# Optimization experiments

Hardware: AMD Instinct MI355X
Metric: run time of the kernel (lower is better)

The kernel has to match this reference:

```python
import jax, jax.numpy as jnp
import numpy as np

N, E, D, H, EDIM, FIN = 16384, 65536, 512, 4, 4, 7
C = D  # per-head out channels (concat=False)


def seg_softmax(logits, seg, n):
    # numerically stable softmax over edges grouped by destination node
    m = jax.ops.segment_max(logits, seg, num_segments=n)
    e = jnp.exp(logits - m[seg])
    s = jax.ops.segment_sum(e, seg, num_segments=n)
    return e / (s[seg] + 1e-16)


def layer_norm(h, g, b):
    mu = h.mean(-1, keepdims=True)
    var = h.var(-1, keepdims=True)
    return (h - mu) / jnp.sqrt(var + 1e-5) * g + b


def setup_inputs() -> dict:
    key = jax.random.key(0)
    ks = jax.random.split(key, 24)
    f32 = jnp.float32
    nrm = lambda k, shp, s=0.05: jax.random.normal(k, shp, dtype=f32) * s
    inp = {}
    inp['x'] = jax.random.normal(ks[0], (N, FIN), dtype=f32)
    inp['edge_index'] = jax.random.randint(ks[1], (2, E), 0, N)
    inp['edge_attr'] = jax.random.uniform(ks[2], (E, EDIM), dtype=f32)
    # input projection
    inp['Wproj'] = nrm(ks[3], (FIN, D)); inp['bproj'] = jnp.zeros((D,), f32)
    # GINEConv (eps=0): edge lin + 2-layer MLP (512->1024->512)
    inp['gine_edge_W'] = nrm(ks[4], (EDIM, D)); inp['gine_edge_b'] = jnp.zeros((D,), f32)
    inp['gine_W1'] = nrm(ks[5], (D, 2 * D)); inp['gine_b1'] = jnp.zeros((2 * D,), f32)
    inp['gine_W2'] = nrm(ks[6], (2 * D, D)); inp['gine_b2'] = jnp.zeros((D,), f32)
    # GATv2Conv heads=4, concat=False
    inp['gat_Wl'] = nrm(ks[7], (D, H * C)); inp['gat_bl'] = jnp.zeros((H * C,), f32)
    inp['gat_Wr'] = nrm(ks[8], (D, H * C)); inp['gat_br'] = jnp.zeros((H * C,), f32)
    inp['gat_edge_W'] = nrm(ks[9], (EDIM, H * C))
    inp['gat_att'] = nrm(ks[10], (H, C))
    inp['gat_bias'] = jnp.zeros((D,), f32)
    # two GCNConv layers
    inp['gcn1_W'] = nrm(ks[11], (D, D)); inp['gcn1_b'] = jnp.zeros((D,), f32)
    inp['gcn2_W'] = nrm(ks[12], (D, D)); inp['gcn2_b'] = jnp.zeros((D,), f32)
    # 4 LayerNorms
    inp['ln_gamma'] = jnp.ones((4, D), f32)
    inp['ln_beta'] = jnp.zeros((4, D), f32)
    return inp


def _forward(x, edge_attr, Wproj, bproj, gine_edge_W, gine_edge_b, gine_W1, gine_b1,
             gine_W2, gine_b2, gat_Wl, gat_bl, gat_Wr, gat_br, gat_edge_W, gat_att,
             gat_bias, gcn1_W, gcn1_b, gcn2_W, gcn2_b, ln_gamma, ln_beta, edge_index):
    n = x.shape[0]
    src, dst = edge_index[0], edge_index[1]
    h = jax.nn.relu(x @ Wproj + bproj)

    # ---- layer 0: GINEConv, sum_j relu(x_j + lin_e(e_ij)), eps=0 ----
    res = h
    e = edge_attr @ gine_edge_W + gine_edge_b                      # [E, D]
    m = jax.nn.relu(h[src] + e)
    agg = jax.ops.segment_sum(m, dst, num_segments=n)              # [N, D]
    g = h + agg
    g = jax.nn.relu(g @ gine_W1 + gine_b1) @ gine_W2 + gine_b2
    h = layer_norm(jax.nn.relu(g) + res, ln_gamma[0], ln_beta[0])

    # ---- layer 1: GATv2Conv (heads=4, concat=False, self-loops, edge_dim=4) ----
    res = h
    loop = jnp.arange(n)
    src2 = jnp.concatenate([src, loop])
    dst2 = jnp.concatenate([dst, loop])
    mean_attr = edge_attr.mean(0)                                  # fill_value='mean'
    eattr2 = jnp.concatenate(
        [edge_attr, jnp.broadcast_to(mean_attr, (n, edge_attr.shape[1]))], 0)
    nh, nc = gat_att.shape
    xl = (h @ gat_Wl + gat_bl).reshape(n, nh, nc)                  # source transform
    xr = (h @ gat_Wr + gat_br).reshape(n, nh, nc)                  # target transform
    ee = (eattr2 @ gat_edge_W).reshape(-1, nh, nc)
    z = jax.nn.leaky_relu(xl[src2] + xr[dst2] + ee, 0.2)           # [E2, H, C]
    logits = jnp.einsum('ehc,hc->eh', z, gat_att)                  # [E2, H]
    alpha = seg_softmax(logits, dst2, n)
    out = jax.ops.segment_sum(xl[src2] * alpha[..., None], dst2, num_segments=n)
    g = out.mean(1) + gat_bias                                     # concat=False -> mean
    h = layer_norm(jax.nn.relu(g) + res, ln_gamma[1], ln_beta[1])

    # ---- layers 2,3: GCNConv (self-loops + symmetric norm) ----
    deg = jax.ops.segment_sum(jnp.ones_like(dst2, dtype=h.dtype), dst2, num_segments=n)
    dinv = jax.lax.rsqrt(deg)
    norm = dinv[src2] * dinv[dst2]
    for i, (W, b) in enumerate(((gcn1_W, gcn1_b), (gcn2_W, gcn2_b)), start=2):
        res = h
        hw = h @ W
        g = jax.ops.segment_sum(hw[src2] * norm[:, None], dst2, num_segments=n) + b
        h = layer_norm(jax.nn.relu(g) + res, ln_gamma[i], ln_beta[i])
    return h


def reference(x, edge_index, edge_attr, Wproj, bproj, gine_edge_W, gine_edge_b,
              gine_W1, gine_b1, gine_W2, gine_b2, gat_Wl, gat_bl, gat_Wr, gat_br,
              gat_edge_W, gat_att, gat_bias, gcn1_W, gcn1_b, gcn2_W, gcn2_b,
              ln_gamma, ln_beta):
    return _forward(x, edge_attr, Wproj, bproj, gine_edge_W, gine_edge_b, gine_W1,
                    gine_b1, gine_W2, gine_b2, gat_Wl, gat_bl, gat_Wr, gat_br,
                    gat_edge_W, gat_att, gat_bias, gcn1_W, gcn1_b, gcn2_W, gcn2_b,
                    ln_gamma, ln_beta, edge_index)
```

## Files before the change

### kernel.cpp

```cpp
#include <hip/hip_runtime.h>
#include <hip/hip_bf16.h>
#include <math.h>

#define NN   16384
#define EE   65536
#define DD   512
#define HH   4
#define FINN 7

typedef __attribute__((ext_vector_type(4))) float  floatx4;
typedef __attribute__((ext_vector_type(8))) float  floatx8;
typedef __attribute__((ext_vector_type(8))) short  shortx8;
typedef __attribute__((ext_vector_type(8))) unsigned short ushortx8;

__device__ inline float bf2f(unsigned short u) {
  return __uint_as_float(((unsigned)u) << 16);
}
__device__ inline unsigned short f2bf(float f) {
  unsigned u = __float_as_uint(f);
  unsigned r = (u + 0x7fffu + ((u >> 16) & 1u)) >> 16;
  return (unsigned short)r;
}
__device__ inline float wave_reduce_sum(float v) {
  #pragma unroll
  for (int off = 32; off > 0; off >>= 1) v += __shfl_down(v, off, 64);
  return v;
}
__device__ inline float wave_allreduce_sum(float v) {
  #pragma unroll
  for (int off = 32; off > 0; off >>= 1) v += __shfl_xor(v, off, 64);
  return v;
}
__device__ inline void async16(const unsigned short* g, unsigned short* l) {
  __builtin_amdgcn_global_load_lds(
      (const __attribute__((address_space(1))) void*)g,
      (__attribute__((address_space(3))) void*)l, 16, 0, 0);
}

__global__ void k_count(const int* __restrict__ dst, int* __restrict__ cnt) {
  int e = blockIdx.x * 256 + threadIdx.x;
  if (e < EE) atomicAdd(&cnt[dst[e]], 1);
}

__global__ void k_scan(const int* __restrict__ cnt, int* __restrict__ offs) {
  __shared__ int sums[256];
  int t = threadIdx.x;
  const int chunk = NN / 256;
  int base = t * chunk;
  int s = 0;
  for (int i = 0; i < chunk; ++i) s += cnt[base + i];
  sums[t] = s;
  __syncthreads();
  for (int off = 1; off < 256; off <<= 1) {
    int v = (t >= off) ? sums[t - off] : 0;
    __syncthreads();
    sums[t] += v;
    __syncthreads();
  }
  int run = (t == 0) ? 0 : sums[t - 1];
  for (int i = 0; i < chunk; ++i) {
    offs[base + i] = run;
    run += cnt[base + i];
  }
  if (t == 255) offs[NN] = run;
}

__global__ void k_fill(const int* __restrict__ dst, const int* __restrict__ offs,
                       int* __restrict__ cursor, int* __restrict__ eids) {
  int e = blockIdx.x * 256 + threadIdx.x;
  if (e >= EE) return;
  int d = dst[e];
  int p = offs[d] + atomicAdd(&cursor[d], 1);
  eids[p] = e;
}

__global__ void k_edge_mean(const float* __restrict__ eattr, float* __restrict__ macc) {
  int tid = blockIdx.x * blockDim.x + threadIdx.x;
  int stride = gridDim.x * blockDim.x;
  float ax = 0.f, ay = 0.f, az = 0.f, aw = 0.f;
  for (int e = tid; e < EE; e += stride) {
    float4 v = ((const float4*)eattr)[e];
    ax += v.x; ay += v.y; az += v.z; aw += v.w;
  }
  ax = wave_reduce_sum(ax); ay = wave_reduce_sum(ay);
  az = wave_reduce_sum(az); aw = wave_reduce_sum(aw);
  if ((threadIdx.x & 63) == 0) {
    atomicAdd(&macc[0], ax); atomicAdd(&macc[1], ay);
    atomicAdd(&macc[2], az); atomicAdd(&macc[3], aw);
  }
}

__global__ void k_transcast(const float* __restrict__ W, int ld,
                            unsigned short* __restrict__ Wt, int K, int N) {
  __shared__ float tile[32][33];
  int bx = blockIdx.x;
  int by = blockIdx.y;
  int tx = threadIdx.x & 31, ty = threadIdx.x >> 5;
  #pragma unroll
  for (int i = 0; i < 32; i += 8)
    tile[ty + i][tx] = W[(size_t)(by * 32 + ty + i) * ld + bx * 32 + tx];
  __syncthreads();
  #pragma unroll
  for (int i = 0; i < 32; i += 8)
    Wt[(size_t)(bx * 32 + ty + i) * K + by * 32 + tx] = f2bf(tile[tx][ty + i]);
}

__global__ void k_bcomb(const float* __restrict__ bl, const float* __restrict__ br,
                        float* __restrict__ bc0, float* __restrict__ bc1) {
  int i = blockIdx.x * 256 + threadIdx.x;
  if (i >= 4096) return;
  int b = i >> 11, c = i & 2047;
  float v = (c < 1024) ? bl[b * 1024 + c] : br[b * 1024 + c - 1024];
  (b ? bc1 : bc0)[c] = v;
}

__global__ void k_proj(const float* __restrict__ x, const float* __restrict__ W,
                       const float* __restrict__ b, unsigned short* __restrict__ hbf) {
  int gid = blockIdx.x * 256 + threadIdx.x;
  if (gid >= NN * DD) return;
  int n = gid >> 9, d = gid & 511;
  const float* xr = x + n * FINN;
  float acc = b[d];
  #pragma unroll
  for (int k = 0; k < FINN; ++k) acc = fmaf(xr[k], W[k * DD + d], acc);
  hbf[gid] = f2bf(fmaxf(acc, 0.f));
}

__global__ __launch_bounds__(256) void k_bgemm(
    const unsigned short* __restrict__ A, const unsigned short* __restrict__ Bt,
    const float* __restrict__ bias, void* __restrict__ Cout,
    int M, int Nc, int K, int act, int outbf) {
  __shared__ unsigned short As[128 * 64];
  __shared__ unsigned short Bs[128 * 64];
  const int tid = threadIdx.x;
  const int wv = tid >> 6;
  const int lane = tid & 63;
  const int row0 = blockIdx.y * 128;
  const int col0 = blockIdx.x * 128;
  const int wrow = (wv & 1) * 64;
  const int wcol = (wv >> 1) * 64;

  floatx4 acc[4][4];
  #pragma unroll
  for (int r = 0; r < 4; ++r)
    #pragma unroll
    for (int c = 0; c < 4; ++c)
      #pragma unroll
      for (int q = 0; q < 4; ++q) acc[r][c][q] = 0.f;

  const unsigned short* Ab = A + (size_t)row0 * K;
  const unsigned short* Bb = Bt + (size_t)col0 * K;
  const int lrow = lane >> 3;
  const int lchunk = (lane & 7) ^ lrow;
  const int lk = lchunk * 8;

  const int frow = lane & 15;
  const int fx = lane >> 4;
  const int fsw = lane & 7;

  for (int k0 = 0; k0 < K; k0 += 64) {
    #pragma unroll
    for (int i = 0; i < 4; ++i) {
      int seg = i * 4 + wv;
      int r = seg * 8 + lrow;
      async16(Ab + (size_t)r * K + k0 + lk, &As[seg * 512]);
      async16(Bb + (size_t)r * K + k0 + lk, &Bs[seg * 512]);
    }
    __syncthreads();
    #pragma unroll
    for (int s = 0; s < 2; ++s) {
      int ch = ((s * 4 + fx) ^ fsw) * 8;
      shortx8 af[4], bfr[4];
      #pragma unroll
      for (int r = 0; r < 4; ++r)
        af[r] = *(const shortx8*)&As[(wrow + r * 16 + frow) * 64 + ch];
      #pragma unroll
      for (int c = 0; c < 4; ++c)
        bfr[c] = *(const shortx8*)&Bs[(wcol + c * 16 + frow) * 64 + ch];
      #pragma unroll
      for (int r = 0; r < 4; ++r)
        #pragma unroll
        for (int c = 0; c < 4; ++c)
          acc[r][c] = __builtin_amdgcn_mfma_f32_16x16x32_bf16(af[r], bfr[c], acc[r][c], 0, 0, 0);
    }
    __syncthreads();
  }

  #pragma unroll
  for (int r = 0; r < 4; ++r) {
    int rowb = row0 + wrow + r * 16 + (lane >> 4) * 4;
    #pragma unroll
    for (int c = 0; c < 4; ++c) {
      int col = col0 + wcol + c * 16 + (lane & 15);
      float bv = bias ? bias[col] : 0.f;
      #pragma unroll
      for (int q = 0; q < 4; ++q) {
        float v = acc[r][c][q] + bv;
        if (act) v = fmaxf(v, 0.f);
        if (outbf)
          ((unsigned short*)Cout)[(size_t)(rowb + q) * Nc + col] = f2bf(v);
        else
          ((float*)Cout)[(size_t)(rowb + q) * Nc + col] = v;
      }
    }
  }
}

__global__ void k_gine_agg(const unsigned short* __restrict__ hbf,
                           const int* __restrict__ src, const float* __restrict__ eattr,
                           const float* __restrict__ geW, const float* __restrict__ geb,
                           const int* __restrict__ offs, const int* __restrict__ eids,
                           unsigned short* __restrict__ gbf) {
  int wave = (blockIdx.x * blockDim.x + threadIdx.x) >> 6;
  int lane = threadIdx.x & 63;
  if (wave >= NN) return;
  int n = wave;
  int cbase = lane * 8;
  floatx8 w0, w1, w2, w3, bb;
  #pragma unroll
  for (int j = 0; j < 8; ++j) {
    bb[j] = geb[cbase + j];
    w0[j] = geW[0 * DD + cbase + j];
    w1[j] = geW[1 * DD + cbase + j];
    w2[j] = geW[2 * DD + cbase + j];
    w3[j] = geW[3 * DD + cbase + j];
  }
  floatx8 acc = {0.f, 0.f, 0.f, 0.f, 0.f, 0.f, 0.f, 0.f};
  int beg = offs[n], end = offs[n + 1];
  int ecur = (beg < end) ? eids[beg] : 0;
  int scur = (beg < end) ? src[ecur] : 0;
  for (int p = beg; p < end; ++p) {
    int e = ecur, s = scur;
    if (p + 1 < end) { ecur = eids[p + 1]; scur = src[ecur]; }
    float4 ea = ((const float4*)eattr)[e];
    ushortx8 hv = *(const ushortx8*)(hbf + (size_t)s * DD + cbase);
    #pragma unroll
    for (int j = 0; j < 8; ++j) {
      float ev = bb[j];
      ev = fmaf(ea.x, w0[j], ev);
      ev = fmaf(ea.y, w1[j], ev);
      ev = fmaf(ea.z, w2[j], ev);
      ev = fmaf(ea.w, w3[j], ev);
      acc[j] += fmaxf(bf2f(hv[j]) + ev, 0.f);
    }
  }
  ushortx8 hn = *(const ushortx8*)(hbf + (size_t)n * DD + cbase);
  ushortx8 o;
  #pragma unroll
  for (int j = 0; j < 8; ++j) o[j] = f2bf(bf2f(hn[j]) + acc[j]);
  *(ushortx8*)(gbf + (size_t)n * DD + cbase) = o;
}

__global__ void k_ln0(const float* __restrict__ g, const unsigned short* __restrict__ res,
                      const float* __restrict__ gamma, const float* __restrict__ beta,
                      unsigned short* __restrict__ obf) {
  int wave = (blockIdx.x * blockDim.x + threadIdx.x) >> 6;
  int lane = threadIdx.x & 63;
  if (wave >= NN) return;
  int n = wave;
  int cbase = lane * 8;
  const float4* g4 = (const float4*)(g + (size_t)n * DD + cbase);
  ushortx8 rv = *(const ushortx8*)(res + (size_t)n * DD + cbase);
  float4 ga = g4[0], gb = g4[1];
  floatx8 v;
  v[0] = ga.x; v[1] = ga.y; v[2] = ga.z; v[3] = ga.w;
  v[4] = gb.x; v[5] = gb.y; v[6] = gb.z; v[7] = gb.w;
  float s = 0.f, sq = 0.f;
  #pragma unroll
  for (int j = 0; j < 8; ++j) {
    float t = fmaxf(v[j], 0.f) + bf2f(rv[j]);
    v[j] = t;
    s += t; sq += t * t;
  }
  s = wave_allreduce_sum(s);
  sq = wave_allreduce_sum(sq);
  float mu = s * (1.f / DD);
  float var = sq * (1.f / DD) - mu * mu;
  float rstd = rsqrtf(var + 1e-5f);
  ushortx8 ob;
  #pragma unroll
  for (int j = 0; j < 8; ++j)
    ob[j] = f2bf(fmaf((v[j] - mu) * rstd, gamma[cbase + j], beta[cbase + j]));
  *(ushortx8*)(obf + (size_t)n * DD + cbase) = ob;
}

__global__ __launch_bounds__(256) void k_gat_fused(
    const unsigned short* __restrict__ xlr,
    const int* __restrict__ src,
    const int* __restrict__ offs, const int* __restrict__ eids,
    const float* __restrict__ eattr, const float* __restrict__ macc,
    const float* __restrict__ geW ,
    const float* __restrict__ att ,
    float* __restrict__ B, unsigned short* __restrict__ Xbf,
    const float* __restrict__ gbias,
    const float* __restrict__ gamma, const float* __restrict__ beta,
    int batch) {
  __shared__ float lsum[2][512];
  int wv = threadIdx.x >> 6;
  int lane = threadIdx.x & 63;
  int slot = wv >> 1;
  int h = wv & 1;
  int n = blockIdx.x * 2 + slot;
  int c8 = lane * 8;
  int hoff = h * 512;
  int hc = (2 * batch + h) * 512 + c8;
  const float invE = 1.f / EE;
  float meax = macc[0] * invE, meay = macc[1] * invE;
  float meaz = macc[2] * invE, meaw = macc[3] * invE;
  int beg = offs[n], end = offs[n + 1];

  floatx8 w0, w1, w2, w3, at, xr;
  #pragma unroll
  for (int j = 0; j < 8; ++j) {
    w0[j] = geW[0 * (HH * DD) + hc + j];
    w1[j] = geW[1 * (HH * DD) + hc + j];
    w2[j] = geW[2 * (HH * DD) + hc + j];
    w3[j] = geW[3 * (HH * DD) + hc + j];
    at[j] = att[hc + j];
  }
  {
    ushortx8 rr = *(const ushortx8*)(xlr + (size_t)n * 2048 + 1024 + hoff + c8);
    #pragma unroll
    for (int j = 0; j < 8; ++j) xr[j] = bf2f(rr[j]);
  }

  float l;
  floatx8 acc;
  {
    ushortx8 a = *(const ushortx8*)(xlr + (size_t)n * 2048 + hoff + c8);
    float z = 0.f;
    #pragma unroll
    for (int j = 0; j < 8; ++j) {
      float t = bf2f(a[j]) + xr[j];
      t = fmaf(meax, w0[j], t);
      t = fmaf(meay, w1[j], t);
      t = fmaf(meaz, w2[j], t);
      t = fmaf(meaw, w3[j], t);
      t = (t >= 0.f) ? t : 0.2f * t;
      z = fmaf(t, at[j], z);
    }
    #pragma unroll
    for (int off = 32; off > 0; off >>= 1) z += __shfl_xor(z, off, 64);
    float w = __expf(z);
    l = w;
    #pragma unroll
    for (int j = 0; j < 8; ++j) acc[j] = w * bf2f(a[j]);
  }
  int ecur = (beg < end) ? eids[beg] : 0;
  int scur = (beg < end) ? src[ecur] : 0;
  for (int p = beg; p < end; ++p) {
    int e = ecur, s = scur;
    if (p + 1 < end) { ecur = eids[p + 1]; scur = src[ecur]; }
    float4 ea = ((const float4*)eattr)[e];
    ushortx8 a = *(const ushortx8*)(xlr + (size_t)s * 2048 + hoff + c8);
    float z = 0.f;
    #pragma unroll
    for (int j = 0; j < 8; ++j) {
      float t = bf2f(a[j]) + xr[j];
      t = fmaf(ea.x, w0[j], t);
      t = fmaf(ea.y, w1[j], t);
      t = fmaf(ea.z, w2[j], t);
      t = fmaf(ea.w, w3[j], t);
      t = (t >= 0.f) ? t : 0.2f * t;
      z = fmaf(t, at[j], z);
    }
    #pragma unroll
    for (int off = 32; off > 0; off >>= 1) z += __shfl_xor(z, off, 64);
    float w = __expf(z);
    l += w;
    #pragma unroll
    for (int j = 0; j < 8; ++j) acc[j] = fmaf(w, bf2f(a[j]), acc[j]);
  }

  float inv = 1.f / (l + 1e-16f);
  if (h) {
    #pragma unroll
    for (int j = 0; j < 8; ++j) lsum[slot][c8 + j] = acc[j] * inv;
  }
  __syncthreads();
  if (h) return;

  floatx8 hsum;
  #pragma unroll
  for (int j = 0; j < 8; ++j) hsum[j] = acc[j] * inv + lsum[slot][c8 + j];

  float* bp = B + (size_t)n * DD + c8;
  if (batch == 0) {
    float4 o0, o1;
    o0.x = hsum[0]; o0.y = hsum[1]; o0.z = hsum[2]; o0.w = hsum[3];
    o1.x = hsum[4]; o1.y = hsum[5]; o1.z = hsum[6]; o1.w = hsum[7];
    ((float4*)bp)[0] = o0;
    ((float4*)bp)[1] = o1;
    return;
  }
  float4 b0 = ((const float4*)bp)[0];
  float4 b1 = ((const float4*)bp)[1];
  floatx8 prev;
  prev[0] = b0.x; prev[1] = b0.y; prev[2] = b0.z; prev[3] = b0.w;
  prev[4] = b1.x; prev[5] = b1.y; prev[6] = b1.z; prev[7] = b1.w;
  ushortx8 rv = *(const ushortx8*)(Xbf + (size_t)n * DD + c8);
  floatx8 v;
  float s = 0.f, sq = 0.f;
  #pragma unroll
  for (int j = 0; j < 8; ++j) {
    float g = (prev[j] + hsum[j]) * 0.25f + gbias[c8 + j];
    float val = fmaxf(g, 0.f) + bf2f(rv[j]);
    v[j] = val;
    s += val; sq += val * val;
  }
  s = wave_allreduce_sum(s);
  sq = wave_allreduce_sum(sq);
  float mu = s * (1.f / DD);
  float var = sq * (1.f / DD) - mu * mu;
  float rstd = rsqrtf(var + 1e-5f);
  ushortx8 ob;
  #pragma unroll
  for (int j = 0; j < 8; ++j)
    ob[j] = f2bf(fmaf((v[j] - mu) * rstd, gamma[c8 + j], beta[c8 + j]));
  *(ushortx8*)(Xbf + (size_t)n * DD + c8) = ob;
}

__global__ void k_dinv(const int* __restrict__ cnt, float* __restrict__ dinv) {
  int n = blockIdx.x * 256 + threadIdx.x;
  if (n < NN) dinv[n] = rsqrtf((float)cnt[n] + 1.0f);
}

__global__ void k_gcn_ln(const unsigned short* __restrict__ hw, const int* __restrict__ src,
                         const int* __restrict__ offs, const int* __restrict__ eids,
                         const float* __restrict__ dinv, const float* __restrict__ bias,
                         const float* __restrict__ gamma, const float* __restrict__ beta,
                         unsigned short* __restrict__ Xbf, float* __restrict__ outf) {
  int wave = (blockIdx.x * blockDim.x + threadIdx.x) >> 6;
  int lane = threadIdx.x & 63;
  if (wave >= NN) return;
  int n = wave;
  int cbase = lane * 8;
  float dn = dinv[n];
  floatx8 acc;
  {
    float wself = dn * dn;
    ushortx8 hv = *(const ushortx8*)(hw + (size_t)n * DD + cbase);
    #pragma unroll
    for (int j = 0; j < 8; ++j) acc[j] = wself * bf2f(hv[j]);
  }
  int beg = offs[n], end = offs[n + 1];
  int ecur = (beg < end) ? eids[beg] : 0;
  int scur = (beg < end) ? src[ecur] : 0;
  for (int p = beg; p < end; ++p) {
    int s = scur;
    if (p + 1 < end) { ecur = eids[p + 1]; scur = src[ecur]; }
    float wgt = dinv[s] * dn;
    ushortx8 hv = *(const ushortx8*)(hw + (size_t)s * DD + cbase);
    #pragma unroll
    for (int j = 0; j < 8; ++j) acc[j] = fmaf(wgt, bf2f(hv[j]), acc[j]);
  }
  ushortx8 rv = *(const ushortx8*)(Xbf + (size_t)n * DD + cbase);
  floatx8 v;
  float s = 0.f, sq = 0.f;
  #pragma unroll
  for (int j = 0; j < 8; ++j) {
    float g = acc[j] + bias[cbase + j];
    float t = fmaxf(g, 0.f) + bf2f(rv[j]);
    v[j] = t;
    s += t; sq += t * t;
  }
  s = wave_allreduce_sum(s);
  sq = wave_allreduce_sum(sq);
  float mu = s * (1.f / DD);
  float var = sq * (1.f / DD) - mu * mu;
  float rstd = rsqrtf(var + 1e-5f);
  if (outf) {
    float4* o4 = (float4*)(outf + (size_t)n * DD + cbase);
    float4 oa, ob4;
    oa.x = fmaf((v[0] - mu) * rstd, gamma[cbase + 0], beta[cbase + 0]);
    oa.y = fmaf((v[1] - mu) * rstd, gamma[cbase + 1], beta[cbase + 1]);
    oa.z = fmaf((v[2] - mu) * rstd, gamma[cbase + 2], beta[cbase + 2]);
    oa.w = fmaf((v[3] - mu) * rstd, gamma[cbase + 3], beta[cbase + 3]);
    ob4.x = fmaf((v[4] - mu) * rstd, gamma[cbase + 4], beta[cbase + 4]);
    ob4.y = fmaf((v[5] - mu) * rstd, gamma[cbase + 5], beta[cbase + 5]);
    ob4.z = fmaf((v[6] - mu) * rstd, gamma[cbase + 6], beta[cbase + 6]);
    ob4.w = fmaf((v[7] - mu) * rstd, gamma[cbase + 7], beta[cbase + 7]);
    o4[0] = oa;
    o4[1] = ob4;
  } else {
    ushortx8 ob;
    #pragma unroll
    for (int j = 0; j < 8; ++j)
      ob[j] = f2bf(fmaf((v[j] - mu) * rstd, gamma[cbase + j], beta[cbase + j]));
    *(ushortx8*)(Xbf + (size_t)n * DD + cbase) = ob;
  }
}

static void launch_bgemm(const unsigned short* A, const unsigned short* Bt,
                         const float* bias, void* C, int M, int Nc, int K,
                         int act, int outbf, hipStream_t stream) {
  dim3 grid(Nc / 128, M / 128);
  k_bgemm<<<grid, 256, 0, stream>>>(A, Bt, bias, C, M, Nc, K, act, outbf);
}

extern "C" void kernel_launch(void* const* d_in, const int* in_sizes, int n_in,
                              void* d_out, int out_size, void* d_ws, size_t ws_size,
                              hipStream_t stream) {
  const float* x       = (const float*)d_in[0];
  const int*   eidx    = (const int*)d_in[1];
  const float* eattr   = (const float*)d_in[2];
  const float* Wproj   = (const float*)d_in[3];
  const float* bproj   = (const float*)d_in[4];
  const float* geW     = (const float*)d_in[5];
  const float* geb     = (const float*)d_in[6];
  const float* gW1     = (const float*)d_in[7];
  const float* gb1     = (const float*)d_in[8];
  const float* gW2     = (const float*)d_in[9];
  const float* gb2     = (const float*)d_in[10];
  const float* gatWl   = (const float*)d_in[11];
  const float* gatbl   = (const float*)d_in[12];
  const float* gatWr   = (const float*)d_in[13];
  const float* gatbr   = (const float*)d_in[14];
  const float* gateW   = (const float*)d_in[15];
  const float* gatatt  = (const float*)d_in[16];
  const float* gatbias = (const float*)d_in[17];
  const float* gcn1W   = (const float*)d_in[18];
  const float* gcn1b   = (const float*)d_in[19];
  const float* gcn2W   = (const float*)d_in[20];
  const float* gcn2b   = (const float*)d_in[21];
  const float* lgamma  = (const float*)d_in[22];
  const float* lbeta   = (const float*)d_in[23];
  const int* srcArr = eidx;
  const int* dstArr = eidx + EE;

  char* p = (char*)d_ws;
  float* B            = (float*)p;          p += (size_t)NN * DD * 4;
  unsigned short* Xbf = (unsigned short*)p; p += (size_t)NN * DD * 2;
  unsigned short* U   = (unsigned short*)p; p += (size_t)NN * 2048 * 2;
  unsigned short* w1t = (unsigned short*)p; p += (size_t)1024 * 512 * 2;
  unsigned short* w2t = (unsigned short*)p; p += (size_t)512 * 1024 * 2;
  unsigned short* wc0 = (unsigned short*)p; p += (size_t)2048 * 512 * 2;
  unsigned short* wc1 = (unsigned short*)p; p += (size_t)2048 * 512 * 2;
  unsigned short* g1t = (unsigned short*)p; p += (size_t)512 * 512 * 2;
  unsigned short* g2t = (unsigned short*)p; p += (size_t)512 * 512 * 2;
  float* bc0      = (float*)p;          p += 2048 * 4;
  float* bc1      = (float*)p;          p += 2048 * 4;
  float* macc     = (float*)p;          p += 4 * 4;
  float* dinv     = (float*)p;          p += (size_t)NN * 4;
  int*   cnt      = (int*)p;            p += (size_t)NN * 4;
  int*   offs     = (int*)p;            p += (size_t)(NN + 1) * 4 + 12;
  int*   cursor   = (int*)p;            p += (size_t)NN * 4;
  int*   eids     = (int*)p;            p += (size_t)EE * 4;

  unsigned short* Zbf = U;
  unsigned short* Ybf = U + (size_t)NN * 512;
  unsigned short* XLR = U;
  unsigned short* hw  = U;

  hipMemsetAsync(cnt, 0, NN * sizeof(int), stream);
  hipMemsetAsync(cursor, 0, NN * sizeof(int), stream);
  hipMemsetAsync(macc, 0, 4 * sizeof(float), stream);

  k_count<<<EE / 256, 256, 0, stream>>>(dstArr, cnt);
  k_scan<<<1, 256, 0, stream>>>(cnt, offs);
  k_fill<<<EE / 256, 256, 0, stream>>>(dstArr, offs, cursor, eids);
  k_edge_mean<<<64, 256, 0, stream>>>(eattr, macc);

  {
    k_transcast<<<dim3(1024 / 32, 512 / 32), 256, 0, stream>>>(gW1, 1024, w1t, 512, 1024);
    k_transcast<<<dim3(512 / 32, 1024 / 32), 256, 0, stream>>>(gW2, 512, w2t, 1024, 512);
    k_transcast<<<dim3(1024 / 32, 512 / 32), 256, 0, stream>>>(gatWl, 2048, wc0, 512, 1024);
    k_transcast<<<dim3(1024 / 32, 512 / 32), 256, 0, stream>>>(gatWr, 2048, wc0 + (size_t)1024 * 512, 512, 1024);
    k_transcast<<<dim3(1024 / 32, 512 / 32), 256, 0, stream>>>(gatWl + 1024, 2048, wc1, 512, 1024);
    k_transcast<<<dim3(1024 / 32, 512 / 32), 256, 0, stream>>>(gatWr + 1024, 2048, wc1 + (size_t)1024 * 512, 512, 1024);
    k_transcast<<<dim3(512 / 32, 512 / 32), 256, 0, stream>>>(gcn1W, 512, g1t, 512, 512);
    k_transcast<<<dim3(512 / 32, 512 / 32), 256, 0, stream>>>(gcn2W, 512, g2t, 512, 512);
    k_bcomb<<<16, 256, 0, stream>>>(gatbl, gatbr, bc0, bc1);
  }

  k_proj<<<NN * DD / 256, 256, 0, stream>>>(x, Wproj, bproj, Xbf);

  k_gine_agg<<<NN / 4, 256, 0, stream>>>(Xbf, srcArr, eattr, geW, geb, offs, eids, Zbf);
  launch_bgemm(Zbf, w1t, gb1, Ybf, NN, 1024, 512, 1, 1, stream);
  launch_bgemm(Ybf, w2t, gb2, B, NN, 512, 1024, 0, 0, stream);
  k_ln0<<<NN / 4, 256, 0, stream>>>(B, Xbf, lgamma, lbeta, Xbf);

  for (int b = 0; b < 2; ++b) {
    launch_bgemm(Xbf, b ? wc1 : wc0, b ? bc1 : bc0, XLR, NN, 2048, 512, 0, 1, stream);
    k_gat_fused<<<NN / 2, 256, 0, stream>>>(XLR, srcArr, offs, eids, eattr, macc,
                                            gateW, gatatt, B, Xbf, gatbias,
                                            lgamma + DD, lbeta + DD, b);
  }

  k_dinv<<<NN / 256, 256, 0, stream>>>(cnt, dinv);
  launch_bgemm(Xbf, g1t, nullptr, hw, NN, 512, 512, 0, 1, stream);
  k_gcn_ln<<<NN / 4, 256, 0, stream>>>(hw, srcArr, offs, eids, dinv, gcn1b,
                                       lgamma + 2 * DD, lbeta + 2 * DD, Xbf, nullptr);
  launch_bgemm(Xbf, g2t, nullptr, hw, NN, 512, 512, 0, 1, stream);
  k_gcn_ln<<<NN / 4, 256, 0, stream>>>(hw, srcArr, offs, eids, dinv, gcn2b,
                                       lgamma + 3 * DD, lbeta + 3 * DD, Xbf, (float*)d_out);
}
```

Measured before the change: 614.9 us.

## Pre-sort edge sources and attributes by destination, swizzle GEMM workgroups

The CSR fill now writes the source index and edge attributes directly in destination-sorted order, and per-edge dinv[src] is precomputed once. This removes the eids→src→eattr double indirection in the GINE, GAT and GCN aggregation loops. The bf16 GEMM also remaps workgroup IDs in groups of 8 when the grid size allows, to change L2/XCD locality. The prefetch reads srcs[p+1] past the segment end, which is covered by padding the buffers; it adds extra scatter writes in the fill kernel.

```diff
diff --git a/kernel.cpp b/kernel.cpp
--- a/kernel.cpp
+++ b/kernel.cpp
@@ -65,13 +65,16 @@
   if (t == 255) offs[NN] = run;
 }
 
-__global__ void k_fill(const int* __restrict__ dst, const int* __restrict__ offs,
-                       int* __restrict__ cursor, int* __restrict__ eids) {
+__global__ void k_fill(const int* __restrict__ dst, const int* __restrict__ src,
+                       const float* __restrict__ eattr, const int* __restrict__ offs,
+                       int* __restrict__ cursor, int* __restrict__ srcs,
+                       float4* __restrict__ ea4) {
   int e = blockIdx.x * 256 + threadIdx.x;
   if (e >= EE) return;
   int d = dst[e];
   int p = offs[d] + atomicAdd(&cursor[d], 1);
-  eids[p] = e;
+  srcs[p] = src[e];
+  ea4[p] = ((const float4*)eattr)[e];
 }
 
 __global__ void k_edge_mean(const float* __restrict__ eattr, float* __restrict__ macc) {
@@ -135,8 +138,15 @@
   const int tid = threadIdx.x;
   const int wv = tid >> 6;
   const int lane = tid & 63;
-  const int row0 = blockIdx.y * 128;
-  const int col0 = blockIdx.x * 128;
+  int gx = gridDim.x;
+  int nwg = gx * gridDim.y;
+  int wg = blockIdx.y * gx + blockIdx.x;
+  if ((nwg & 7) == 0) {
+    int cpx = nwg >> 3;
+    wg = (wg & 7) * cpx + (wg >> 3);
+  }
+  const int row0 = (wg / gx) * 128;
+  const int col0 = (wg % gx) * 128;
   const int wrow = (wv & 1) * 64;
   const int wcol = (wv >> 1) * 64;
 
@@ -207,9 +217,9 @@
 }
 
 __global__ void k_gine_agg(const unsigned short* __restrict__ hbf,
-                           const int* __restrict__ src, const float* __restrict__ eattr,
+                           const int* __restrict__ srcs, const float4* __restrict__ ea4,
                            const float* __restrict__ geW, const float* __restrict__ geb,
-                           const int* __restrict__ offs, const int* __restrict__ eids,
+                           const int* __restrict__ offs,
                            unsigned short* __restrict__ gbf) {
   int wave = (blockIdx.x * blockDim.x + threadIdx.x) >> 6;
   int lane = threadIdx.x & 63;
@@ -227,12 +237,11 @@
   }
   floatx8 acc = {0.f, 0.f, 0.f, 0.f, 0.f, 0.f, 0.f, 0.f};
   int beg = offs[n], end = offs[n + 1];
-  int ecur = (beg < end) ? eids[beg] : 0;
-  int scur = (beg < end) ? src[ecur] : 0;
+  int scur = srcs[beg];
   for (int p = beg; p < end; ++p) {
-    int e = ecur, s = scur;
-    if (p + 1 < end) { ecur = eids[p + 1]; scur = src[ecur]; }
-    float4 ea = ((const float4*)eattr)[e];
+    int s = scur;
+    scur = srcs[p + 1];
+    float4 ea = ea4[p];
     ushortx8 hv = *(const ushortx8*)(hbf + (size_t)s * DD + cbase);
     #pragma unroll
     for (int j = 0; j < 8; ++j) {
@@ -286,9 +295,9 @@
 
 __global__ __launch_bounds__(256) void k_gat_fused(
     const unsigned short* __restrict__ xlr,
-    const int* __restrict__ src,
-    const int* __restrict__ offs, const int* __restrict__ eids,
-    const float* __restrict__ eattr, const float* __restrict__ macc,
+    const int* __restrict__ srcs,
+    const int* __restrict__ offs, const float4* __restrict__ ea4,
+    const float* __restrict__ macc,
     const float* __restrict__ geW ,
     const float* __restrict__ att ,
     float* __restrict__ B, unsigned short* __restrict__ Xbf,
@@ -346,12 +355,11 @@
     #pragma unroll
     for (int j = 0; j < 8; ++j) acc[j] = w * bf2f(a[j]);
   }
-  int ecur = (beg < end) ? eids[beg] : 0;
-  int scur = (beg < end) ? src[ecur] : 0;
+  int scur = srcs[beg];
   for (int p = beg; p < end; ++p) {
-    int e = ecur, s = scur;
-    if (p + 1 < end) { ecur = eids[p + 1]; scur = src[ecur]; }
-    float4 ea = ((const float4*)eattr)[e];
+    int s = scur;
+    scur = srcs[p + 1];
+    float4 ea = ea4[p];
     ushortx8 a = *(const ushortx8*)(xlr + (size_t)s * 2048 + hoff + c8);
     float z = 0.f;
     #pragma unroll
@@ -425,8 +433,14 @@
   if (n < NN) dinv[n] = rsqrtf((float)cnt[n] + 1.0f);
 }
 
-__global__ void k_gcn_ln(const unsigned short* __restrict__ hw, const int* __restrict__ src,
-                         const int* __restrict__ offs, const int* __restrict__ eids,
+__global__ void k_dsrc(const int* __restrict__ srcs, const float* __restrict__ dinv,
+                       float* __restrict__ dinv_src) {
+  int p = blockIdx.x * 256 + threadIdx.x;
+  if (p < EE) dinv_src[p] = dinv[srcs[p]];
+}
+
+__global__ void k_gcn_ln(const unsigned short* __restrict__ hw, const int* __restrict__ srcs,
+                         const int* __restrict__ offs, const float* __restrict__ dinv_src,
                          const float* __restrict__ dinv, const float* __restrict__ bias,
                          const float* __restrict__ gamma, const float* __restrict__ beta,
                          unsigned short* __restrict__ Xbf, float* __restrict__ outf) {
@@ -444,12 +458,11 @@
     for (int j = 0; j < 8; ++j) acc[j] = wself * bf2f(hv[j]);
   }
   int beg = offs[n], end = offs[n + 1];
-  int ecur = (beg < end) ? eids[beg] : 0;
-  int scur = (beg < end) ? src[ecur] : 0;
+  int scur = srcs[beg];
   for (int p = beg; p < end; ++p) {
     int s = scur;
-    if (p + 1 < end) { ecur = eids[p + 1]; scur = src[ecur]; }
-    float wgt = dinv[s] * dn;
+    scur = srcs[p + 1];
+    float wgt = dinv_src[p] * dn;
     ushortx8 hv = *(const ushortx8*)(hw + (size_t)s * DD + cbase);
     #pragma unroll
     for (int j = 0; j < 8; ++j) acc[j] = fmaf(wgt, bf2f(hv[j]), acc[j]);
@@ -538,14 +551,16 @@
   unsigned short* wc1 = (unsigned short*)p; p += (size_t)2048 * 512 * 2;
   unsigned short* g1t = (unsigned short*)p; p += (size_t)512 * 512 * 2;
   unsigned short* g2t = (unsigned short*)p; p += (size_t)512 * 512 * 2;
+  float4* ea4     = (float4*)p;         p += (size_t)(EE + 4) * 16;
   float* bc0      = (float*)p;          p += 2048 * 4;
   float* bc1      = (float*)p;          p += 2048 * 4;
   float* macc     = (float*)p;          p += 4 * 4;
   float* dinv     = (float*)p;          p += (size_t)NN * 4;
+  float* dinv_src = (float*)p;          p += (size_t)(EE + 16) * 4;
   int*   cnt      = (int*)p;            p += (size_t)NN * 4;
   int*   offs     = (int*)p;            p += (size_t)(NN + 1) * 4 + 12;
   int*   cursor   = (int*)p;            p += (size_t)NN * 4;
-  int*   eids     = (int*)p;            p += (size_t)EE * 4;
+  int*   srcs     = (int*)p;            p += (size_t)(EE + 16) * 4;
 
   unsigned short* Zbf = U;
   unsigned short* Ybf = U + (size_t)NN * 512;
@@ -558,7 +573,9 @@
 
   k_count<<<EE / 256, 256, 0, stream>>>(dstArr, cnt);
   k_scan<<<1, 256, 0, stream>>>(cnt, offs);
-  k_fill<<<EE / 256, 256, 0, stream>>>(dstArr, offs, cursor, eids);
+  k_fill<<<EE / 256, 256, 0, stream>>>(dstArr, srcArr, eattr, offs, cursor, srcs, ea4);
+  k_dinv<<<NN / 256, 256, 0, stream>>>(cnt, dinv);
+  k_dsrc<<<EE / 256, 256, 0, stream>>>(srcs, dinv, dinv_src);
   k_edge_mean<<<64, 256, 0, stream>>>(eattr, macc);
 
   {
@@ -575,23 +592,22 @@
 
   k_proj<<<NN * DD / 256, 256, 0, stream>>>(x, Wproj, bproj, Xbf);
 
-  k_gine_agg<<<NN / 4, 256, 0, stream>>>(Xbf, srcArr, eattr, geW, geb, offs, eids, Zbf);
+  k_gine_agg<<<NN / 4, 256, 0, stream>>>(Xbf, srcs, ea4, geW, geb, offs, Zbf);
   launch_bgemm(Zbf, w1t, gb1, Ybf, NN, 1024, 512, 1, 1, stream);
   launch_bgemm(Ybf, w2t, gb2, B, NN, 512, 1024, 0, 0, stream);
   k_ln0<<<NN / 4, 256, 0, stream>>>(B, Xbf, lgamma, lbeta, Xbf);
 
   for (int b = 0; b < 2; ++b) {
     launch_bgemm(Xbf, b ? wc1 : wc0, b ? bc1 : bc0, XLR, NN, 2048, 512, 0, 1, stream);
-    k_gat_fused<<<NN / 2, 256, 0, stream>>>(XLR, srcArr, offs, eids, eattr, macc,
+    k_gat_fused<<<NN / 2, 256, 0, stream>>>(XLR, srcs, offs, ea4, macc,
                                             gateW, gatatt, B, Xbf, gatbias,
                                             lgamma + DD, lbeta + DD, b);
   }
 
-  k_dinv<<<NN / 256, 256, 0, stream>>>(cnt, dinv);
   launch_bgemm(Xbf, g1t, nullptr, hw, NN, 512, 512, 0, 1, stream);
-  k_gcn_ln<<<NN / 4, 256, 0, stream>>>(hw, srcArr, offs, eids, dinv, gcn1b,
+  k_gcn_ln<<<NN / 4, 256, 0, stream>>>(hw, srcs, offs, dinv_src, dinv, gcn1b,
                                        lgamma + 2 * DD, lbeta + 2 * DD, Xbf, nullptr);
   launch_bgemm(Xbf, g2t, nullptr, hw, NN, 512, 512, 0, 1, stream);
-  k_gcn_ln<<<NN / 4, 256, 0, stream>>>(hw, srcArr, offs, eids, dinv, gcn2b,
+  k_gcn_ln<<<NN / 4, 256, 0, stream>>>(hw, srcs, offs, dinv_src, dinv, gcn2b,
                                        lgamma + 3 * DD, lbeta + 3 * DD, Xbf, (float*)d_out);
 }
```

After: 588.4 us. 4.3% less time.
